# Kernel tuning notes

Hardware: AMD Instinct MI355X
Metric: run time of the kernel (lower is better)

## Reference

```python
import jax, jax.numpy as jnp
import numpy as np

D_MODEL, H, D_K, D_V, D_FF = 1024, 16, 64, 64, 4096
B, L = 2, 2048
EPS = 1e-5


def layer_norm(x, g, b):
    mu = jnp.mean(x, axis=-1, keepdims=True)
    var = jnp.mean(jnp.square(x - mu), axis=-1, keepdims=True)
    return (x - mu) * jax.lax.rsqrt(var + EPS) * g + b


def setup_inputs() -> dict:
    key = jax.random.key(0)
    ks = jax.random.split(key, 12)
    s = 0.02
    x = jax.random.normal(ks[0], (B, L, D_MODEL), dtype=jnp.float32)
    Wq = jax.random.normal(ks[1], (H, D_MODEL, D_K), dtype=jnp.float32) * s
    Wk = jax.random.normal(ks[2], (H, D_MODEL, D_K), dtype=jnp.float32) * s
    Wv = jax.random.normal(ks[3], (H, D_MODEL, D_V), dtype=jnp.float32) * s
    bq = jnp.zeros((H, D_K), dtype=jnp.float32)
    bk = jnp.zeros((H, D_K), dtype=jnp.float32)
    bv = jnp.zeros((H, D_V), dtype=jnp.float32)
    Wo = jax.random.normal(ks[4], (H * D_V, D_MODEL), dtype=jnp.float32) * s
    W1 = jax.random.normal(ks[5], (D_MODEL, D_FF), dtype=jnp.float32) * s
    b1 = jnp.zeros((D_FF,), dtype=jnp.float32)
    W2 = jax.random.normal(ks[6], (D_FF, D_MODEL), dtype=jnp.float32) * s
    ln1_g = jnp.ones((D_MODEL,), dtype=jnp.float32)
    ln1_b = jnp.zeros((D_MODEL,), dtype=jnp.float32)
    ln2_g = jnp.ones((D_MODEL,), dtype=jnp.float32)
    ln2_b = jnp.zeros((D_MODEL,), dtype=jnp.float32)
    return dict(x=x, Wq=Wq, bq=bq, Wk=Wk, bk=bk, Wv=Wv, bv=bv, Wo=Wo,
                ln1_g=ln1_g, ln1_b=ln1_b, W1=W1, b1=b1, W2=W2,
                ln2_g=ln2_g, ln2_b=ln2_b)


def reference(x, Wq, bq, Wk, bk, Wv, bv, Wo, ln1_g, ln1_b, W1, b1, W2, ln2_g, ln2_b):
    # Batched multi-head attention (all heads at once, equivalent to the
    # per-head Python loop in the original module).
    Q = jnp.einsum('bld,hdk->bhlk', x, Wq) + bq[None, :, None, :]
    K = jnp.einsum('bld,hdk->bhlk', x, Wk) + bk[None, :, None, :]
    V = jnp.einsum('bld,hdv->bhlv', x, Wv) + bv[None, :, None, :]
    scores = jnp.einsum('bhlk,bhmk->bhlm', Q, K) * (1.0 / jnp.sqrt(jnp.float32(D_K)))
    attn = jax.nn.softmax(scores, axis=-1)
    O = jnp.einsum('bhlm,bhmv->bhlv', attn, V)        # [b,h,l,dv]
    O = jnp.transpose(O, (0, 2, 1, 3)).reshape(x.shape[0], x.shape[1], H * D_V)
    mha = O @ Wo                                       # [b,l,d_model]
    # residual + LayerNorm (dropout_prob=0 -> identity)
    h1 = layer_norm(x + mha, ln1_g, ln1_b)
    ff = jax.nn.relu(h1 @ W1 + b1) @ W2
    return layer_norm(h1 + ff, ln2_g, ln2_b)
```

## Files before the change

### kernel.cpp

```cpp
#include <hip/hip_runtime.h>

typedef unsigned short u16;
typedef unsigned int u32;
typedef short bf16x8 __attribute__((ext_vector_type(8)));
typedef float f32x4 __attribute__((ext_vector_type(4)));
typedef unsigned int u32x2 __attribute__((ext_vector_type(2)));

#define D_MODEL 1024
#define NH 16
#define DK 64
#define DFF 4096
#define BATCH 2
#define SEQ 2048
#define BL (BATCH*SEQ)
#define NQKV 3072

__device__ __forceinline__ float bfraw2f(u16 u) {
    union { u32 i; float f; } c; c.i = ((u32)u) << 16; return c.f;
}
__device__ __forceinline__ u16 f2bfraw(float f) {
    union { float f; u32 i; } c; c.f = f;
    u32 i = c.i;
    u32 lsb = (i >> 16) & 1u;
    i += 0x7fffu + lsb;
    return (u16)(i >> 16);
}
__device__ __forceinline__ u32 fasu(float f) {
    union { float f; u32 i; } c; c.f = f; return c.i;
}
__device__ __forceinline__ u32 pack_bf2(float lo, float hi) {
    return __builtin_amdgcn_perm(fasu(hi) + 0x8000u, fasu(lo) + 0x8000u,
                                 0x07060302u);
}
__device__ __forceinline__ void gload_lds16(const u16* g, u16* l) {
    __builtin_amdgcn_global_load_lds(
        (const __attribute__((address_space(1))) void*)g,
        (__attribute__((address_space(3))) void*)l, 16, 0, 0);
}

__global__ __launch_bounds__(256) void cast_f32_bf16(const float* __restrict__ in,
                                                     u16* __restrict__ out) {
    int i = (blockIdx.x * 256 + threadIdx.x) * 4;
    f32x4 v = *(const f32x4*)&in[i];
#pragma unroll
    for (int j = 0; j < 4; j++) out[i + j] = f2bfraw(v[j]);
}


__global__ __launch_bounds__(256) void transpose2d(const float* __restrict__ in,
                                                   u16* __restrict__ out,
                                                   int R, int C) {
    __shared__ u16 t[64][65];
    int c0 = blockIdx.x * 64, r0 = blockIdx.y * 64;
    int col = threadIdx.x & 63, rr = threadIdx.x >> 6;
    for (int i = rr; i < 64; i += 4)
        t[i][col] = f2bfraw(in[(size_t)(r0 + i) * C + c0 + col]);
    __syncthreads();
    for (int i = rr; i < 64; i += 4)
        out[(size_t)(c0 + i) * R + r0 + col] = t[col][i];
}

__global__ __launch_bounds__(256) void transpose_wqkv(const float* __restrict__ Wq,
                                                      const float* __restrict__ Wk,
                                                      const float* __restrict__ Wv,
                                                      u16* __restrict__ out) {
    __shared__ u16 t[64][65];
    int d0 = blockIdx.x * 64;
    int h = blockIdx.y;
    int ms = blockIdx.z;
    const float* W = (ms == 0) ? Wq : (ms == 1) ? Wk : Wv;
    const float* src = W + (size_t)h * D_MODEL * DK;
    int col = threadIdx.x & 63, rr = threadIdx.x >> 6;
    for (int i = rr; i < 64; i += 4)
        t[i][col] = f2bfraw(src[(size_t)(d0 + i) * DK + col]);
    __syncthreads();
    u16* dst = out + (size_t)(ms * 1024 + h * 64) * D_MODEL;
    for (int i = rr; i < 64; i += 4)
        dst[(size_t)i * D_MODEL + d0 + col] = t[col][i];
}

__global__ __launch_bounds__(256) void transpose_v(const u16* __restrict__ qkv,
                                                   u16* __restrict__ vt) {
    __shared__ u16 t[64][65];
    int l0 = blockIdx.x * 64;
    int h = blockIdx.y;
    int b = blockIdx.z;
    int col = threadIdx.x & 63, rr = threadIdx.x >> 6;
    const u16* src = qkv + (size_t)(b * SEQ) * NQKV + 2048 + h * 64;
    for (int i = rr; i < 64; i += 4)
        t[i][col] = src[(size_t)(l0 + i) * NQKV + col];
    __syncthreads();
    u16* dst = vt + (size_t)((b * NH + h) * 64) * SEQ;
    for (int i = rr; i < 64; i += 4)
        dst[(size_t)i * SEQ + l0 + col] = t[col][i];
}

__global__ __launch_bounds__(256) void concat_bias(const float* __restrict__ bq,
                                                   const float* __restrict__ bk,
                                                   const float* __restrict__ bv,
                                                   float* __restrict__ out) {
    int i = blockIdx.x * 256 + threadIdx.x;
    out[i] = (i < 1024) ? bq[i] : (i < 2048) ? bk[i - 1024] : bv[i - 2048];
}


template <int OUT_F32, int RELU, int HASBIAS, int SPLITK>
__global__ __launch_bounds__(256, 4) void gemm_bt(const u16* __restrict__ A,
                                                  const u16* __restrict__ Bt,
                                                  const float* __restrict__ bias,
                                                  void* __restrict__ Cout,
                                                  int M, int N, int K) {
    __shared__ __attribute__((aligned(16))) u16 As[128 * 64];
    __shared__ __attribute__((aligned(16))) u16 Bs[128 * 64];
    const int tid = threadIdx.x;
    const int lane = tid & 63, wid = tid >> 6;
    const int quad = lane >> 4, l16 = lane & 15;
    const int m0 = blockIdx.x * 128, n0 = blockIdx.y * 128;
    const int z = (SPLITK > 1) ? blockIdx.z : 0;
    const int Klen = K / SPLITK;
    const int kend = (z + 1) * Klen;
    const int wm = (wid >> 1) * 64, wn = (wid & 1) * 64;

    f32x4 acc[4][4];
#pragma unroll
    for (int i = 0; i < 4; i++)
#pragma unroll
        for (int j = 0; j < 4; j++) acc[i][j] = (f32x4){0.f, 0.f, 0.f, 0.f};

    const int srow = lane >> 3, scol = (lane & 7) * 8;

    for (int kb = z * Klen; kb < kend; kb += 64) {
#pragma unroll
        for (int p = 0; p < 4; p++) {
            int c = wid * 4 + p;
            int row = c * 8 + srow;
            gload_lds16(&A[(size_t)(m0 + row) * K + kb + scol], &As[c * 512]);
            gload_lds16(&Bt[(size_t)(n0 + row) * K + kb + scol], &Bs[c * 512]);
        }
        __syncthreads();
#pragma unroll
        for (int kh = 0; kh < 2; kh++) {
            bf16x8 af[4], bf[4];
#pragma unroll
            for (int t = 0; t < 4; t++) {
                af[t] = *(const bf16x8*)&As[(wm + t * 16 + l16) * 64 + kh * 32 + quad * 8];
                bf[t] = *(const bf16x8*)&Bs[(wn + t * 16 + l16) * 64 + kh * 32 + quad * 8];
            }
#pragma unroll
            for (int i = 0; i < 4; i++)
#pragma unroll
                for (int j = 0; j < 4; j++)
                    acc[i][j] = __builtin_amdgcn_mfma_f32_16x16x32_bf16(
                        af[i], bf[j], acc[i][j], 0, 0, 0);
        }
        __syncthreads();
    }

    float* outf = (float*)Cout + (size_t)z * M * N;
#pragma unroll
    for (int i = 0; i < 4; i++) {
#pragma unroll
        for (int j = 0; j < 4; j++) {
#pragma unroll
            for (int r = 0; r < 4; r++) {
                int row = m0 + wm + i * 16 + quad * 4 + r;
                int col = n0 + wn + j * 16 + l16;
                float v = acc[i][j][r];
                if (HASBIAS) v += bias[col];
                if (RELU) v = v > 0.f ? v : 0.f;
                if (OUT_F32)
                    outf[(size_t)row * N + col] = v;
                else
                    ((u16*)Cout)[(size_t)row * N + col] = f2bfraw(v);
            }
        }
    }
}

__global__ __launch_bounds__(256, 2) void attn_kernel(const u16* __restrict__ qkv,
                                                      const u16* __restrict__ vt,
                                                      u16* __restrict__ O) {
    constexpr int LDK = 72;
    constexpr int LDV = 136;
    constexpr int LDP = 136;
    __shared__ __attribute__((aligned(16))) u16 Ks[128 * LDK];
    __shared__ __attribute__((aligned(16))) u16 Vs[64 * LDV];
    __shared__ __attribute__((aligned(16))) u16 Ps[4][32 * LDP];

    const int tid = threadIdx.x;
    const int lane = tid & 63, wid = tid >> 6;
    const int quad = lane >> 4, l16 = lane & 15;
    const int b = blockIdx.z, h = blockIdx.y;
    const int q0 = blockIdx.x * 128 + wid * 32;

    bf16x8 qf[2][2];
#pragma unroll
    for (int qt = 0; qt < 2; qt++) {
        const size_t qrow = (size_t)(b * SEQ + q0 + qt * 16 + l16) * NQKV + h * DK;
        qf[qt][0] = *(const bf16x8*)&qkv[qrow + quad * 8];
        qf[qt][1] = *(const bf16x8*)&qkv[qrow + 32 + quad * 8];
    }
    const u16* Kbase = qkv + (size_t)(b * SEQ) * NQKV + D_MODEL + h * DK;
    const u16* Vbase = vt + (size_t)((b * NH + h) * DK) * SEQ;

    f32x4 oacc[4][2];
#pragma unroll
    for (int d = 0; d < 4; d++) {
        oacc[d][0] = (f32x4){0.f, 0.f, 0.f, 0.f};
        oacc[d][1] = (f32x4){0.f, 0.f, 0.f, 0.f};
    }
    float lr[2] = {0.f, 0.f};
    const float scale = 0.125f;
    const f32x4 Z = {0.f, 0.f, 0.f, 0.f};

    for (int kt = 0; kt < SEQ; kt += 128) {
        bf16x8 kreg[4], vreg[4];
#pragma unroll
        for (int p = 0; p < 4; p++) {
            int s = p * 256 + tid;
            kreg[p] = *(const bf16x8*)&Kbase[(size_t)(kt + (s >> 3)) * NQKV + (s & 7) * 8];
            vreg[p] = *(const bf16x8*)&Vbase[(size_t)(s >> 4) * SEQ + kt + (s & 15) * 8];
        }
#pragma unroll
        for (int p = 0; p < 4; p++) {
            int s = p * 256 + tid;
            *(bf16x8*)&Ks[(s >> 3) * LDK + (s & 7) * 8] = kreg[p];
            *(bf16x8*)&Vs[(s >> 4) * LDV + (s & 15) * 8] = vreg[p];
        }
        __syncthreads();

        f32x4 sacc[8][2];
#pragma unroll
        for (int nt = 0; nt < 8; nt++) {
            const u16* kr = &Ks[(nt * 16 + l16) * LDK];
            bf16x8 kf0 = *(const bf16x8*)&kr[quad * 8];
            bf16x8 kf1 = *(const bf16x8*)&kr[32 + quad * 8];
#pragma unroll
            for (int qt = 0; qt < 2; qt++) {
                f32x4 s0 = __builtin_amdgcn_mfma_f32_16x16x32_bf16(kf0, qf[qt][0], Z, 0, 0, 0);
                sacc[nt][qt] = __builtin_amdgcn_mfma_f32_16x16x32_bf16(kf1, qf[qt][1], s0, 0, 0, 0);
            }
        }

#pragma unroll
        for (int qt = 0; qt < 2; qt++) {
            u16* prow = &Ps[wid][(qt * 16 + l16) * LDP];
#pragma unroll
            for (int nt = 0; nt < 8; nt++) {
                float p0 = __expf(sacc[nt][qt][0] * scale);
                float p1 = __expf(sacc[nt][qt][1] * scale);
                float p2 = __expf(sacc[nt][qt][2] * scale);
                float p3 = __expf(sacc[nt][qt][3] * scale);
                lr[qt] += (p0 + p1) + (p2 + p3);
                u32x2 w;
                w.x = pack_bf2(p0, p1);
                w.y = pack_bf2(p2, p3);
                *(u32x2*)&prow[nt * 16 + quad * 4] = w;
            }
        }

#pragma unroll
        for (int ks = 0; ks < 4; ks++) {
            bf16x8 pf0 = *(const bf16x8*)&Ps[wid][l16 * LDP + ks * 32 + quad * 8];
            bf16x8 pf1 = *(const bf16x8*)&Ps[wid][(16 + l16) * LDP + ks * 32 + quad * 8];
#pragma unroll
            for (int d = 0; d < 4; d++) {
                bf16x8 vf = *(const bf16x8*)&Vs[(d * 16 + l16) * LDV + ks * 32 + quad * 8];
                oacc[d][0] = __builtin_amdgcn_mfma_f32_16x16x32_bf16(vf, pf0, oacc[d][0], 0, 0, 0);
                oacc[d][1] = __builtin_amdgcn_mfma_f32_16x16x32_bf16(vf, pf1, oacc[d][1], 0, 0, 0);
            }
        }
        __syncthreads();
    }

#pragma unroll
    for (int qt = 0; qt < 2; qt++) {
        lr[qt] += __shfl_xor(lr[qt], 16, 64);
        lr[qt] += __shfl_xor(lr[qt], 32, 64);
    }

#pragma unroll
    for (int qt = 0; qt < 2; qt++) {
        float iv = 1.f / lr[qt];
        size_t row = (size_t)(b * SEQ + q0 + qt * 16 + l16);
#pragma unroll
        for (int d = 0; d < 4; d++) {
            float o0 = oacc[d][qt][0] * iv, o1 = oacc[d][qt][1] * iv;
            float o2 = oacc[d][qt][2] * iv, o3 = oacc[d][qt][3] * iv;
            u32x2 w;
            w.x = ((u32)f2bfraw(o1) << 16) | f2bfraw(o0);
            w.y = ((u32)f2bfraw(o3) << 16) | f2bfraw(o2);
            *(u32x2*)&O[row * D_MODEL + h * DK + d * 16 + quad * 4] = w;
        }
    }
}

__global__ __launch_bounds__(256) void ln3_kernel(const float* __restrict__ xa,
                                                  const float* __restrict__ xb,
                                                  const float* __restrict__ xc,
                                                  const float* __restrict__ g,
                                                  const float* __restrict__ be,
                                                  u16* __restrict__ out_bf,
                                                  float* __restrict__ out_f) {
    int row = blockIdx.x;
    int tid = threadIdx.x;
    const float* pa = xa + (size_t)row * D_MODEL;
    const float* pb = xb + (size_t)row * D_MODEL;
    const float* pc = xc + (size_t)row * D_MODEL;
    int c = tid * 4;
    f32x4 av = *(const f32x4*)&pa[c];
    f32x4 bv = *(const f32x4*)&pb[c];
    f32x4 cv = *(const f32x4*)&pc[c];
    float v[4];
    float s = 0.f, ss = 0.f;
#pragma unroll
    for (int i = 0; i < 4; i++) {
        v[i] = av[i] + bv[i] + cv[i];
        s += v[i];
        ss += v[i] * v[i];
    }
#pragma unroll
    for (int off = 32; off; off >>= 1) {
        s += __shfl_down(s, off, 64);
        ss += __shfl_down(ss, off, 64);
    }
    __shared__ float red[8];
    int wid = tid >> 6, lane = tid & 63;
    if (lane == 0) { red[wid] = s; red[4 + wid] = ss; }
    __syncthreads();
    if (tid == 0) {
        red[0] = red[0] + red[1] + red[2] + red[3];
        red[4] = red[4] + red[5] + red[6] + red[7];
    }
    __syncthreads();
    float mu = red[0] * (1.f / D_MODEL);
    float var = red[4] * (1.f / D_MODEL) - mu * mu;
    float rs = rsqrtf(var + 1e-5f);
#pragma unroll
    for (int i = 0; i < 4; i++) {
        float o = (v[i] - mu) * rs * g[c + i] + be[c + i];
        if (out_f) out_f[(size_t)row * D_MODEL + c + i] = o;
        if (out_bf) out_bf[(size_t)row * D_MODEL + c + i] = f2bfraw(o);
    }
}

extern "C" void kernel_launch(void* const* d_in, const int* in_sizes, int n_in,
                              void* d_out, int out_size, void* d_ws, size_t ws_size,
                              hipStream_t stream) {
    const float* x   = (const float*)d_in[0];
    const float* Wq  = (const float*)d_in[1];
    const float* bq  = (const float*)d_in[2];
    const float* Wk  = (const float*)d_in[3];
    const float* bk  = (const float*)d_in[4];
    const float* Wv  = (const float*)d_in[5];
    const float* bv  = (const float*)d_in[6];
    const float* Wo  = (const float*)d_in[7];
    const float* g1  = (const float*)d_in[8];
    const float* be1 = (const float*)d_in[9];
    const float* W1  = (const float*)d_in[10];
    const float* b1  = (const float*)d_in[11];
    const float* W2  = (const float*)d_in[12];
    const float* g2  = (const float*)d_in[13];
    const float* be2 = (const float*)d_in[14];

    char* w = (char*)d_ws;
    auto alloc = [&](size_t bytes) {
        char* p = w;
        w += (bytes + 255) & ~(size_t)255;
        return p;
    };
    u16* wqkv_t = (u16*)alloc((size_t)NQKV * D_MODEL * 2);
    u16* wo_t   = (u16*)alloc((size_t)D_MODEL * D_MODEL * 2);
    u16* w1_t   = (u16*)alloc((size_t)DFF * D_MODEL * 2);
    u16* w2_t   = (u16*)alloc((size_t)D_MODEL * DFF * 2);
    float* bqkv = (float*)alloc((size_t)NQKV * 4);
    u16* x_bf   = (u16*)alloc((size_t)BL * D_MODEL * 2);
    u16* qkvbuf = (u16*)alloc((size_t)BL * NQKV * 2);
    u16* vtbuf  = (u16*)alloc((size_t)BATCH * NH * DK * SEQ * 2);
    u16* obuf   = (u16*)alloc((size_t)BL * D_MODEL * 2);
    float* mha_p = (float*)alloc((size_t)2 * BL * D_MODEL * 4);
    u16* h1_bf  = (u16*)alloc((size_t)BL * D_MODEL * 2);
    float* h1_f = (float*)alloc((size_t)BL * D_MODEL * 4);
    u16* ffa    = (u16*)alloc((size_t)BL * DFF * 2);
    float* ffb_p = (float*)alloc((size_t)2 * BL * D_MODEL * 4);

    cast_f32_bf16<<<dim3(BL * D_MODEL / 1024), 256, 0, stream>>>(x, x_bf);
    transpose_wqkv<<<dim3(16, 16, 3), 256, 0, stream>>>(Wq, Wk, Wv, wqkv_t);
    transpose2d<<<dim3(16, 16), 256, 0, stream>>>(Wo, wo_t, 1024, 1024);
    transpose2d<<<dim3(64, 16), 256, 0, stream>>>(W1, w1_t, 1024, 4096);
    transpose2d<<<dim3(16, 64), 256, 0, stream>>>(W2, w2_t, 4096, 1024);
    concat_bias<<<dim3(12), 256, 0, stream>>>(bq, bk, bv, bqkv);

    gemm_bt<0, 0, 1, 1><<<dim3(32, 24), 256, 0, stream>>>(x_bf, wqkv_t, bqkv,
                                                          qkvbuf, BL, NQKV, D_MODEL);
    transpose_v<<<dim3(32, 16, 2), 256, 0, stream>>>(qkvbuf, vtbuf);
    attn_kernel<<<dim3(16, 16, 2), 256, 0, stream>>>(qkvbuf, vtbuf, obuf);
    gemm_bt<1, 0, 0, 2><<<dim3(32, 8, 2), 256, 0, stream>>>(obuf, wo_t, nullptr,
                                                            mha_p, BL, D_MODEL, D_MODEL);
    ln3_kernel<<<dim3(BL), 256, 0, stream>>>(x, mha_p, mha_p + (size_t)BL * D_MODEL,
                                             g1, be1, h1_bf, h1_f);
    gemm_bt<0, 1, 1, 1><<<dim3(32, 32), 256, 0, stream>>>(h1_bf, w1_t, b1, ffa,
                                                          BL, DFF, D_MODEL);
    gemm_bt<1, 0, 0, 2><<<dim3(32, 8, 2), 256, 0, stream>>>(ffa, w2_t, nullptr,
                                                            ffb_p, BL, D_MODEL, DFF);
    ln3_kernel<<<dim3(BL), 256, 0, stream>>>(h1_f, ffb_p, ffb_p + (size_t)BL * D_MODEL,
                                             g2, be2, nullptr, (float*)d_out);
}
```

Measured before the change: 389.2 us.

## Fold softmax scale into Q projection, direct-to-LDS K loads, V from global

The QKV GEMM epilogue now multiplies Q columns by scale*log2(e), so the attention kernel can use exp2f without a per-element multiply. K tiles are staged with a direct global-to-LDS load helper, and the V shared-memory tile is removed: V fragments are read straight from global memory inside the PV loop. Less LDS use lets launch bounds move to 3 blocks per CU. The trade is uncoalesced, latency-exposed global V reads in the inner MFMA loop, and unpadded K rows that may cause LDS bank conflicts.

Result: slower. 446.7 us (+14.8%).

```diff
diff --git a/kernel.cpp b/kernel.cpp
--- a/kernel.cpp
+++ b/kernel.cpp
@@ -14,6 +14,7 @@
 #define SEQ 2048
 #define BL (BATCH*SEQ)
 #define NQKV 3072
+#define Q_SCALE 0.18033688011f
 
 __device__ __forceinline__ float bfraw2f(u16 u) {
     union { u32 i; float f; } c; c.i = ((u32)u) << 16; return c.f;
@@ -104,7 +105,7 @@
 }
 
 
-template <int OUT_F32, int RELU, int HASBIAS, int SPLITK>
+template <int OUT_F32, int RELU, int HASBIAS, int SPLITK, int SCALEQ>
 __global__ __launch_bounds__(256, 4) void gemm_bt(const u16* __restrict__ A,
                                                   const u16* __restrict__ Bt,
                                                   const float* __restrict__ bias,
@@ -168,6 +169,7 @@
                 float v = acc[i][j][r];
                 if (HASBIAS) v += bias[col];
                 if (RELU) v = v > 0.f ? v : 0.f;
+                if (SCALEQ && col < 1024) v *= Q_SCALE;
                 if (OUT_F32)
                     outf[(size_t)row * N + col] = v;
                 else
@@ -177,14 +179,11 @@
     }
 }
 
-__global__ __launch_bounds__(256, 2) void attn_kernel(const u16* __restrict__ qkv,
+__global__ __launch_bounds__(256, 3) void attn_kernel(const u16* __restrict__ qkv,
                                                       const u16* __restrict__ vt,
                                                       u16* __restrict__ O) {
-    constexpr int LDK = 72;
-    constexpr int LDV = 136;
     constexpr int LDP = 136;
-    __shared__ __attribute__((aligned(16))) u16 Ks[128 * LDK];
-    __shared__ __attribute__((aligned(16))) u16 Vs[64 * LDV];
+    __shared__ __attribute__((aligned(16))) u16 Ks[128 * 64];
     __shared__ __attribute__((aligned(16))) u16 Ps[4][32 * LDP];
 
     const int tid = threadIdx.x;
@@ -203,6 +202,8 @@
     const u16* Kbase = qkv + (size_t)(b * SEQ) * NQKV + D_MODEL + h * DK;
     const u16* Vbase = vt + (size_t)((b * NH + h) * DK) * SEQ;
 
+    const int srow = lane >> 3, scol = (lane & 7) * 8;
+
     f32x4 oacc[4][2];
 #pragma unroll
     for (int d = 0; d < 4; d++) {
@@ -210,29 +211,21 @@
         oacc[d][1] = (f32x4){0.f, 0.f, 0.f, 0.f};
     }
     float lr[2] = {0.f, 0.f};
-    const float scale = 0.125f;
     const f32x4 Z = {0.f, 0.f, 0.f, 0.f};
 
     for (int kt = 0; kt < SEQ; kt += 128) {
-        bf16x8 kreg[4], vreg[4];
 #pragma unroll
         for (int p = 0; p < 4; p++) {
-            int s = p * 256 + tid;
-            kreg[p] = *(const bf16x8*)&Kbase[(size_t)(kt + (s >> 3)) * NQKV + (s & 7) * 8];
-            vreg[p] = *(const bf16x8*)&Vbase[(size_t)(s >> 4) * SEQ + kt + (s & 15) * 8];
-        }
-#pragma unroll
-        for (int p = 0; p < 4; p++) {
-            int s = p * 256 + tid;
-            *(bf16x8*)&Ks[(s >> 3) * LDK + (s & 7) * 8] = kreg[p];
-            *(bf16x8*)&Vs[(s >> 4) * LDV + (s & 15) * 8] = vreg[p];
+            int c = wid * 4 + p;
+            gload_lds16(&Kbase[(size_t)(kt + c * 8 + srow) * NQKV + scol],
+                        &Ks[c * 512]);
         }
         __syncthreads();
 
         f32x4 sacc[8][2];
 #pragma unroll
         for (int nt = 0; nt < 8; nt++) {
-            const u16* kr = &Ks[(nt * 16 + l16) * LDK];
+            const u16* kr = &Ks[(nt * 16 + l16) * 64];
             bf16x8 kf0 = *(const bf16x8*)&kr[quad * 8];
             bf16x8 kf1 = *(const bf16x8*)&kr[32 + quad * 8];
 #pragma unroll
@@ -247,10 +240,10 @@
             u16* prow = &Ps[wid][(qt * 16 + l16) * LDP];
 #pragma unroll
             for (int nt = 0; nt < 8; nt++) {
-                float p0 = __expf(sacc[nt][qt][0] * scale);
-                float p1 = __expf(sacc[nt][qt][1] * scale);
-                float p2 = __expf(sacc[nt][qt][2] * scale);
-                float p3 = __expf(sacc[nt][qt][3] * scale);
+                float p0 = exp2f(sacc[nt][qt][0]);
+                float p1 = exp2f(sacc[nt][qt][1]);
+                float p2 = exp2f(sacc[nt][qt][2]);
+                float p3 = exp2f(sacc[nt][qt][3]);
                 lr[qt] += (p0 + p1) + (p2 + p3);
                 u32x2 w;
                 w.x = pack_bf2(p0, p1);
@@ -265,7 +258,8 @@
             bf16x8 pf1 = *(const bf16x8*)&Ps[wid][(16 + l16) * LDP + ks * 32 + quad * 8];
 #pragma unroll
             for (int d = 0; d < 4; d++) {
-                bf16x8 vf = *(const bf16x8*)&Vs[(d * 16 + l16) * LDV + ks * 32 + quad * 8];
+                bf16x8 vf = *(const bf16x8*)&Vbase[(size_t)(d * 16 + l16) * SEQ +
+                                                   kt + ks * 32 + quad * 8];
                 oacc[d][0] = __builtin_amdgcn_mfma_f32_16x16x32_bf16(vf, pf0, oacc[d][0], 0, 0, 0);
                 oacc[d][1] = __builtin_amdgcn_mfma_f32_16x16x32_bf16(vf, pf1, oacc[d][1], 0, 0, 0);
             }
@@ -391,18 +385,18 @@
     transpose2d<<<dim3(16, 64), 256, 0, stream>>>(W2, w2_t, 4096, 1024);
     concat_bias<<<dim3(12), 256, 0, stream>>>(bq, bk, bv, bqkv);
 
-    gemm_bt<0, 0, 1, 1><<<dim3(32, 24), 256, 0, stream>>>(x_bf, wqkv_t, bqkv,
-                                                          qkvbuf, BL, NQKV, D_MODEL);
+    gemm_bt<0, 0, 1, 1, 1><<<dim3(32, 24), 256, 0, stream>>>(x_bf, wqkv_t, bqkv,
+                                                             qkvbuf, BL, NQKV, D_MODEL);
     transpose_v<<<dim3(32, 16, 2), 256, 0, stream>>>(qkvbuf, vtbuf);
     attn_kernel<<<dim3(16, 16, 2), 256, 0, stream>>>(qkvbuf, vtbuf, obuf);
-    gemm_bt<1, 0, 0, 2><<<dim3(32, 8, 2), 256, 0, stream>>>(obuf, wo_t, nullptr,
-                                                            mha_p, BL, D_MODEL, D_MODEL);
+    gemm_bt<1, 0, 0, 2, 0><<<dim3(32, 8, 2), 256, 0, stream>>>(obuf, wo_t, nullptr,
+                                                               mha_p, BL, D_MODEL, D_MODEL);
     ln3_kernel<<<dim3(BL), 256, 0, stream>>>(x, mha_p, mha_p + (size_t)BL * D_MODEL,
                                              g1, be1, h1_bf, h1_f);
-    gemm_bt<0, 1, 1, 1><<<dim3(32, 32), 256, 0, stream>>>(h1_bf, w1_t, b1, ffa,
-                                                          BL, DFF, D_MODEL);
-    gemm_bt<1, 0, 0, 2><<<dim3(32, 8, 2), 256, 0, stream>>>(ffa, w2_t, nullptr,
-                                                            ffb_p, BL, D_MODEL, DFF);
+    gemm_bt<0, 1, 1, 1, 0><<<dim3(32, 32), 256, 0, stream>>>(h1_bf, w1_t, b1, ffa,
+                                                             BL, DFF, D_MODEL);
+    gemm_bt<1, 0, 0, 2, 0><<<dim3(32, 8, 2), 256, 0, stream>>>(ffa, w2_t, nullptr,
+                                                               ffb_p, BL, D_MODEL, DFF);
     ln3_kernel<<<dim3(BL), 256, 0, stream>>>(h1_f, ffb_p, ffb_p + (size_t)BL * D_MODEL,
                                              g2, be2, nullptr, (float*)d_out);
 }
```

## Fold softmax scale into QKV GEMM and process attention query tiles sequentially

Applied to the files above, without the earlier changes.

The softmax scale times log2(e) is folded into the Q columns in the QKV GEMM epilogue, so attention can use exp2f directly with no per-element multiply. The attention inner loop now handles the two 16-row query tiles one at a time, which halves the score accumulator registers and the P shared-memory buffer. Launch bounds are raised from 2 to 3 blocks per CU to use the freed resources. In exchange K fragments are reloaded from LDS once per query tile, and Q is stored pre-scaled in bf16, which slightly changes rounding.

Result: slower. 403.3 us (+3.6%).

```diff
diff --git a/kernel.cpp b/kernel.cpp
--- a/kernel.cpp
+++ b/kernel.cpp
@@ -14,6 +14,7 @@
 #define SEQ 2048
 #define BL (BATCH*SEQ)
 #define NQKV 3072
+#define Q_SCALE 0.18033688011f
 
 __device__ __forceinline__ float bfraw2f(u16 u) {
     union { u32 i; float f; } c; c.i = ((u32)u) << 16; return c.f;
@@ -104,7 +105,7 @@
 }
 
 
-template <int OUT_F32, int RELU, int HASBIAS, int SPLITK>
+template <int OUT_F32, int RELU, int HASBIAS, int SPLITK, int SCALEQ>
 __global__ __launch_bounds__(256, 4) void gemm_bt(const u16* __restrict__ A,
                                                   const u16* __restrict__ Bt,
                                                   const float* __restrict__ bias,
@@ -168,6 +169,7 @@
                 float v = acc[i][j][r];
                 if (HASBIAS) v += bias[col];
                 if (RELU) v = v > 0.f ? v : 0.f;
+                if (SCALEQ && col < 1024) v *= Q_SCALE;
                 if (OUT_F32)
                     outf[(size_t)row * N + col] = v;
                 else
@@ -177,7 +179,7 @@
     }
 }
 
-__global__ __launch_bounds__(256, 2) void attn_kernel(const u16* __restrict__ qkv,
+__global__ __launch_bounds__(256, 3) void attn_kernel(const u16* __restrict__ qkv,
                                                       const u16* __restrict__ vt,
                                                       u16* __restrict__ O) {
     constexpr int LDK = 72;
@@ -185,7 +187,7 @@
     constexpr int LDP = 136;
     __shared__ __attribute__((aligned(16))) u16 Ks[128 * LDK];
     __shared__ __attribute__((aligned(16))) u16 Vs[64 * LDV];
-    __shared__ __attribute__((aligned(16))) u16 Ps[4][32 * LDP];
+    __shared__ __attribute__((aligned(16))) u16 Ps[4][16 * LDP];
 
     const int tid = threadIdx.x;
     const int lane = tid & 63, wid = tid >> 6;
@@ -210,7 +212,6 @@
         oacc[d][1] = (f32x4){0.f, 0.f, 0.f, 0.f};
     }
     float lr[2] = {0.f, 0.f};
-    const float scale = 0.125f;
     const f32x4 Z = {0.f, 0.f, 0.f, 0.f};
 
     for (int kt = 0; kt < SEQ; kt += 128) {
@@ -229,45 +230,40 @@
         }
         __syncthreads();
 
-        f32x4 sacc[8][2];
-#pragma unroll
-        for (int nt = 0; nt < 8; nt++) {
-            const u16* kr = &Ks[(nt * 16 + l16) * LDK];
-            bf16x8 kf0 = *(const bf16x8*)&kr[quad * 8];
-            bf16x8 kf1 = *(const bf16x8*)&kr[32 + quad * 8];
-#pragma unroll
-            for (int qt = 0; qt < 2; qt++) {
+#pragma unroll
+        for (int qt = 0; qt < 2; qt++) {
+            f32x4 sacc[8];
+#pragma unroll
+            for (int nt = 0; nt < 8; nt++) {
+                const u16* kr = &Ks[(nt * 16 + l16) * LDK];
+                bf16x8 kf0 = *(const bf16x8*)&kr[quad * 8];
+                bf16x8 kf1 = *(const bf16x8*)&kr[32 + quad * 8];
                 f32x4 s0 = __builtin_amdgcn_mfma_f32_16x16x32_bf16(kf0, qf[qt][0], Z, 0, 0, 0);
-                sacc[nt][qt] = __builtin_amdgcn_mfma_f32_16x16x32_bf16(kf1, qf[qt][1], s0, 0, 0, 0);
+                sacc[nt] = __builtin_amdgcn_mfma_f32_16x16x32_bf16(kf1, qf[qt][1], s0, 0, 0, 0);
             }
-        }
-
-#pragma unroll
-        for (int qt = 0; qt < 2; qt++) {
-            u16* prow = &Ps[wid][(qt * 16 + l16) * LDP];
+
+            u16* prow = &Ps[wid][l16 * LDP];
 #pragma unroll
             for (int nt = 0; nt < 8; nt++) {
-                float p0 = __expf(sacc[nt][qt][0] * scale);
-                float p1 = __expf(sacc[nt][qt][1] * scale);
-                float p2 = __expf(sacc[nt][qt][2] * scale);
-                float p3 = __expf(sacc[nt][qt][3] * scale);
+                float p0 = exp2f(sacc[nt][0]);
+                float p1 = exp2f(sacc[nt][1]);
+                float p2 = exp2f(sacc[nt][2]);
+                float p3 = exp2f(sacc[nt][3]);
                 lr[qt] += (p0 + p1) + (p2 + p3);
                 u32x2 w;
                 w.x = pack_bf2(p0, p1);
                 w.y = pack_bf2(p2, p3);
                 *(u32x2*)&prow[nt * 16 + quad * 4] = w;
             }
-        }
-
-#pragma unroll
-        for (int ks = 0; ks < 4; ks++) {
-            bf16x8 pf0 = *(const bf16x8*)&Ps[wid][l16 * LDP + ks * 32 + quad * 8];
-            bf16x8 pf1 = *(const bf16x8*)&Ps[wid][(16 + l16) * LDP + ks * 32 + quad * 8];
-#pragma unroll
-            for (int d = 0; d < 4; d++) {
-                bf16x8 vf = *(const bf16x8*)&Vs[(d * 16 + l16) * LDV + ks * 32 + quad * 8];
-                oacc[d][0] = __builtin_amdgcn_mfma_f32_16x16x32_bf16(vf, pf0, oacc[d][0], 0, 0, 0);
-                oacc[d][1] = __builtin_amdgcn_mfma_f32_16x16x32_bf16(vf, pf1, oacc[d][1], 0, 0, 0);
+
+#pragma unroll
+            for (int ks = 0; ks < 4; ks++) {
+                bf16x8 pf = *(const bf16x8*)&Ps[wid][l16 * LDP + ks * 32 + quad * 8];
+#pragma unroll
+                for (int d = 0; d < 4; d++) {
+                    bf16x8 vf = *(const bf16x8*)&Vs[(d * 16 + l16) * LDV + ks * 32 + quad * 8];
+                    oacc[d][qt] = __builtin_amdgcn_mfma_f32_16x16x32_bf16(vf, pf, oacc[d][qt], 0, 0, 0);
+                }
             }
         }
         __syncthreads();
@@ -391,18 +387,18 @@
     transpose2d<<<dim3(16, 64), 256, 0, stream>>>(W2, w2_t, 4096, 1024);
     concat_bias<<<dim3(12), 256, 0, stream>>>(bq, bk, bv, bqkv);
 
-    gemm_bt<0, 0, 1, 1><<<dim3(32, 24), 256, 0, stream>>>(x_bf, wqkv_t, bqkv,
-                                                          qkvbuf, BL, NQKV, D_MODEL);
+    gemm_bt<0, 0, 1, 1, 1><<<dim3(32, 24), 256, 0, stream>>>(x_bf, wqkv_t, bqkv,
+                                                             qkvbuf, BL, NQKV, D_MODEL);
     transpose_v<<<dim3(32, 16, 2), 256, 0, stream>>>(qkvbuf, vtbuf);
     attn_kernel<<<dim3(16, 16, 2), 256, 0, stream>>>(qkvbuf, vtbuf, obuf);
-    gemm_bt<1, 0, 0, 2><<<dim3(32, 8, 2), 256, 0, stream>>>(obuf, wo_t, nullptr,
-                                                            mha_p, BL, D_MODEL, D_MODEL);
+    gemm_bt<1, 0, 0, 2, 0><<<dim3(32, 8, 2), 256, 0, stream>>>(obuf, wo_t, nullptr,
+                                                               mha_p, BL, D_MODEL, D_MODEL);
     ln3_kernel<<<dim3(BL), 256, 0, stream>>>(x, mha_p, mha_p + (size_t)BL * D_MODEL,
                                              g1, be1, h1_bf, h1_f);
-    gemm_bt<0, 1, 1, 1><<<dim3(32, 32), 256, 0, stream>>>(h1_bf, w1_t, b1, ffa,
-                                                          BL, DFF, D_MODEL);
-    gemm_bt<1, 0, 0, 2><<<dim3(32, 8, 2), 256, 0, stream>>>(ffa, w2_t, nullptr,
-                                                            ffb_p, BL, D_MODEL, DFF);
+    gemm_bt<0, 1, 1, 1, 0><<<dim3(32, 32), 256, 0, stream>>>(h1_bf, w1_t, b1, ffa,
+                                                             BL, DFF, D_MODEL);
+    gemm_bt<1, 0, 0, 2, 0><<<dim3(32, 8, 2), 256, 0, stream>>>(ffa, w2_t, nullptr,
+                                                               ffb_p, BL, D_MODEL, DFF);
     ln3_kernel<<<dim3(BL), 256, 0, stream>>>(h1_f, ffb_p, ffb_p + (size_t)BL * D_MODEL,
                                              g2, be2, nullptr, (float*)d_out);
 }
```
